# Kernel optimization log

Hardware: AMD Instinct MI355X
Metric: run time of the kernel (lower is better)

Reference implementation:

```python
import jax, jax.numpy as jnp
import numpy as np

D_MODEL = 1024
D_FF = 1024
NUM_EXPERTS = 8
TOP_K = 2


def setup_inputs() -> dict:
    key = jax.random.key(0)
    ks = jax.random.split(key, 5)
    s_in = 1.0 / np.sqrt(D_MODEL)
    s_ff = 1.0 / np.sqrt(D_FF)
    return {
        "x": jax.random.normal(ks[0], (4, 2048, D_MODEL), dtype=jnp.float32),
        "gate_w": jax.random.normal(ks[1], (NUM_EXPERTS, D_MODEL), dtype=jnp.float32) * s_in,
        # torch Linear weight layout: [out_features, in_features], stacked over experts
        "w_gate": jax.random.normal(ks[2], (NUM_EXPERTS, D_FF, D_MODEL), dtype=jnp.float32) * s_in,
        "w_up": jax.random.normal(ks[3], (NUM_EXPERTS, D_FF, D_MODEL), dtype=jnp.float32) * s_in,
        "w_down": jax.random.normal(ks[4], (NUM_EXPERTS, D_MODEL, D_FF), dtype=jnp.float32) * s_ff,
    }


def reference(x, gate_w, w_gate, w_up, w_down):
    B, S, D = x.shape
    T = B * S
    E = gate_w.shape[0]
    xt = x.reshape(T, D)

    # Router
    logits = xt @ gate_w.T                      # [T, E]
    probs = jax.nn.softmax(logits, axis=-1)
    top_v, top_i = jax.lax.top_k(probs, TOP_K)  # [T, K]
    top_v = top_v / jnp.sum(top_v, axis=-1, keepdims=True)

    tokens_per_expert = jnp.sum(jax.nn.one_hot(top_i, E, dtype=jnp.float32), axis=(0, 1))  # [E]
    f = tokens_per_expert / jnp.sum(tokens_per_expert)
    P = jnp.mean(probs, axis=0)
    aux_loss = E * jnp.sum(f * P)

    # Combine weights: per-token weight for each expert (sum over top-k slots)
    combine = jnp.zeros((T, E), dtype=x.dtype).at[jnp.arange(T)[:, None], top_i].add(top_v)  # [T, E]

    # Dense per-expert SwiGLU (equivalent math to masked gather/scatter loop)
    g = jnp.einsum('td,efd->etf', xt, w_gate)   # [E, T, F]
    u = jnp.einsum('td,efd->etf', xt, w_up)     # [E, T, F]
    act = jax.nn.silu(g) * u
    eo = jnp.einsum('etf,edf->etd', act, w_down)  # [E, T, D]

    out = jnp.einsum('te,etd->td', combine, eo).reshape(B, S, D)
    return out, aux_loss, tokens_per_expert
```

## Files before the change

### kernel.cpp

```cpp
#include <hip/hip_runtime.h>


#define T_TOK   8192
#define DM      1024
#define DFF     1024
#define NE      8
#define CAP     16384
#define R1_BLK  (T_TOK / 4)
#define CVT_BLK 2048

typedef __attribute__((ext_vector_type(8))) short bf16x8;
typedef __attribute__((ext_vector_type(4))) float f32x4;

#define ASYNC16(gp, lp) __builtin_amdgcn_global_load_lds( \
    (const __attribute__((address_space(1))) unsigned int*)(gp), \
    (__attribute__((address_space(3))) unsigned int*)(lp), 16, 0, 0)

__device__ __forceinline__ unsigned short f2bf(float f) {
    union { float f; unsigned u; } c; c.f = f;
    unsigned r = c.u + 0x7fffu + ((c.u >> 16) & 1u);
    return (unsigned short)(r >> 16);
}
__device__ __forceinline__ float bf2f(unsigned short h) {
    union { unsigned u; float f; } c; c.u = ((unsigned)h) << 16;
    return c.f;
}

__global__ __launch_bounds__(256) void pre_kernel(
    const float* __restrict__ x, const float* __restrict__ gate_w,
    const float* __restrict__ s0, const float* __restrict__ s1, const float* __restrict__ s2,
    unsigned short* __restrict__ d0, unsigned short* __restrict__ d1, unsigned short* __restrict__ d2,
    unsigned short* __restrict__ xb,
    int* __restrict__ topi, float2* __restrict__ topw, float* __restrict__ psum_part)
{
    int tid = threadIdx.x;

    if (blockIdx.x >= R1_BLK) {
        int base = (blockIdx.x - R1_BLK) * 256 + tid;
        #pragma unroll
        for (int it = 0; it < 12; ++it) {
            int idx = base + it * (CVT_BLK * 256);
            int seg = idx >> 21;
            int off = (idx & ((1 << 21) - 1)) * 4;
            const float* s = (seg == 0) ? s0 : (seg == 1) ? s1 : s2;
            unsigned short* d = (seg == 0) ? d0 : (seg == 1) ? d1 : d2;
            float4 v = *(const float4*)(s + off);
            ushort4 o;
            o.x = f2bf(v.x); o.y = f2bf(v.y); o.z = f2bf(v.z); o.w = f2bf(v.w);
            *(ushort4*)(d + off) = o;
        }
        return;
    }

    __shared__ float gw[NE * DM];
    __shared__ float blk_psum[NE];

    for (int i = tid; i < NE * DM; i += 256) gw[i] = gate_w[i];
    if (tid < NE) blk_psum[tid] = 0.f;
    __syncthreads();

    int wv = tid >> 6, lane = tid & 63;
    int t = blockIdx.x * 4 + wv;

    float acc[NE];
    #pragma unroll
    for (int e = 0; e < NE; ++e) acc[e] = 0.f;
    const float* xr = x + (size_t)t * DM;
    unsigned short* xbr = xb + (size_t)t * DM;
    #pragma unroll 4
    for (int i = 0; i < DM / 64; ++i) {
        float xv = xr[i * 64 + lane];
        xbr[i * 64 + lane] = f2bf(xv);
        #pragma unroll
        for (int e = 0; e < NE; ++e)
            acc[e] += xv * gw[e * DM + i * 64 + lane];
    }
    #pragma unroll
    for (int e = 0; e < NE; ++e) {
        float v = acc[e];
        #pragma unroll
        for (int s = 32; s > 0; s >>= 1) v += __shfl_xor(v, s, 64);
        acc[e] = v;
    }
    if (lane == 0) {
        float mx = acc[0];
        #pragma unroll
        for (int e = 1; e < NE; ++e) mx = fmaxf(mx, acc[e]);
        float p[NE], sum = 0.f;
        #pragma unroll
        for (int e = 0; e < NE; ++e) { p[e] = expf(acc[e] - mx); sum += p[e]; }
        float inv = 1.f / sum;
        #pragma unroll
        for (int e = 0; e < NE; ++e) { p[e] *= inv; atomicAdd(&blk_psum[e], p[e]); }
        int i1 = 0; float v1 = p[0];
        #pragma unroll
        for (int e = 1; e < NE; ++e) if (p[e] > v1) { v1 = p[e]; i1 = e; }
        int i2 = -1; float v2 = -1.f;
        #pragma unroll
        for (int e = 0; e < NE; ++e) { if (e == i1) continue; if (p[e] > v2) { v2 = p[e]; i2 = e; } }
        float winv = 1.f / (v1 + v2);
        topi[t] = i1 | (i2 << 8);
        topw[t] = make_float2(v1 * winv, v2 * winv);
    }
    __syncthreads();
    if (tid < NE) psum_part[blockIdx.x * NE + tid] = blk_psum[tid];
}

__global__ __launch_bounds__(1024) void scatfin_kernel(
    const int* __restrict__ topi, const float* __restrict__ psum_part,
    int* __restrict__ elist, int* __restrict__ ecnt, float* __restrict__ out_tail)
{
    __shared__ int lcnt[NE], rbase[NE], cb8[NE];
    __shared__ float parts[NE];
    __shared__ float red[1024];
    int tid = threadIdx.x;

    if (tid < NE) rbase[tid] = 0;
    __syncthreads();
    #pragma unroll
    for (int ch = 0; ch < T_TOK / 1024; ++ch) {
        int tt = ch * 1024 + tid;
        int pk = topi[tt];
        int e1 = pk & 0xff, e2 = (pk >> 8) & 0xff;
        if (tid < NE) lcnt[tid] = 0;
        __syncthreads();
        int p1 = atomicAdd(&lcnt[e1], 1);
        int p2 = atomicAdd(&lcnt[e2], 1);
        __syncthreads();
        if (tid < NE) { cb8[tid] = rbase[tid]; rbase[tid] += lcnt[tid]; }
        __syncthreads();
        elist[e1 * CAP + cb8[e1] + p1] = tt * 2 + 0;
        elist[e2 * CAP + cb8[e2] + p2] = tt * 2 + 1;
        __syncthreads();
    }
    if (tid < NE) ecnt[tid] = rbase[tid];

    int e = tid & 7, b0 = tid >> 3;
    float s = 0.f;
    for (int b = b0; b < R1_BLK; b += 128) s += psum_part[b * NE + e];
    red[tid] = s;
    __syncthreads();
    if (tid < NE) {
        float tot = 0.f;
        #pragma unroll
        for (int j = 0; j < 128; ++j) tot += red[tid + NE * j];
        float P = tot / (float)T_TOK;
        float f = (float)rbase[tid] / (float)(2 * T_TOK);
        parts[tid] = f * P;
        out_tail[1 + tid] = (float)rbase[tid];
    }
    __syncthreads();
    if (tid == 0) {
        float s2 = 0.f;
        for (int i = 0; i < NE; ++i) s2 += parts[i];
        out_tail[0] = (float)NE * s2;
    }
}

__global__ __launch_bounds__(256) void gemm1_kernel(
    const unsigned short* __restrict__ xb,
    const unsigned short* __restrict__ wgb,
    const unsigned short* __restrict__ wub,
    const int* __restrict__ elist, const int* __restrict__ ecnt,
    unsigned short* __restrict__ Hbuf)
{
    int e = blockIdx.z, mt = blockIdx.y, ft = blockIdx.x;
    int ne = ecnt[e];
    if (mt * 128 >= ne) return;

    __shared__ unsigned short As[128 * 64];
    __shared__ unsigned short Gs[64 * 64];
    __shared__ unsigned short Us[64 * 64];
    __shared__ int tsafe[128];
    __shared__ int rawts[128];

    int tid = threadIdx.x;
    if (tid < 128) {
        int pos = mt * 128 + tid;
        int ts0 = elist[e * CAP + mt * 128];
        int ts = (pos < ne) ? elist[e * CAP + pos] : ts0;
        tsafe[tid] = ts >> 1;
        rawts[tid] = (pos < ne) ? ts : -1;
    }
    __syncthreads();

    int wave = tid >> 6, lane = tid & 63;
    int quad = lane >> 4, col = lane & 15;
    int cr = tid >> 3;
    int cl = ((tid & 7) ^ (cr & 7)) * 8;

    const size_t woff = (size_t)e * (size_t)DFF * DM;
    const unsigned short* ap[4];
    #pragma unroll
    for (int j = 0; j < 4; ++j) ap[j] = xb + (size_t)tsafe[j * 32 + cr] * DM + cl;
    const unsigned short* gp[2];
    const unsigned short* up[2];
    #pragma unroll
    for (int j = 0; j < 2; ++j) {
        gp[j] = wgb + woff + (size_t)(ft * 64 + j * 32 + cr) * DM + cl;
        up[j] = wub + woff + (size_t)(ft * 64 + j * 32 + cr) * DM + cl;
    }
    unsigned short* lA = As + wave * 512;
    unsigned short* lG = Gs + wave * 512;
    unsigned short* lU = Us + wave * 512;

    f32x4 accG[2][4], accU[2][4];
    #pragma unroll
    for (int i = 0; i < 2; ++i)
        #pragma unroll
        for (int n = 0; n < 4; ++n) { accG[i][n] = (f32x4){0,0,0,0}; accU[i][n] = (f32x4){0,0,0,0}; }

    for (int k0 = 0; k0 < DM; k0 += 64) {
        __syncthreads();
        #pragma unroll
        for (int j = 0; j < 4; ++j) ASYNC16(ap[j] + k0, lA + j * 2048);
        #pragma unroll
        for (int j = 0; j < 2; ++j) {
            ASYNC16(gp[j] + k0, lG + j * 2048);
            ASYNC16(up[j] + k0, lU + j * 2048);
        }
        __syncthreads();
        #pragma unroll
        for (int ksoff = 0; ksoff < 8; ksoff += 4) {
            bf16x8 a[2], g[4], u[4];
            #pragma unroll
            for (int i = 0; i < 2; ++i) {
                int m = wave * 32 + i * 16 + col;
                a[i] = *(const bf16x8*)&As[m * 64 + ((quad + ksoff) ^ (m & 7)) * 8];
            }
            #pragma unroll
            for (int n = 0; n < 4; ++n) {
                int nb = n * 16 + col;
                int off = nb * 64 + ((quad + ksoff) ^ (nb & 7)) * 8;
                g[n] = *(const bf16x8*)&Gs[off];
                u[n] = *(const bf16x8*)&Us[off];
            }
            #pragma unroll
            for (int i = 0; i < 2; ++i)
                #pragma unroll
                for (int n = 0; n < 4; ++n) {
                    accG[i][n] = __builtin_amdgcn_mfma_f32_16x16x32_bf16(a[i], g[n], accG[i][n], 0, 0, 0);
                    accU[i][n] = __builtin_amdgcn_mfma_f32_16x16x32_bf16(a[i], u[n], accU[i][n], 0, 0, 0);
                }
        }
    }
    #pragma unroll
    for (int i = 0; i < 2; ++i) {
        #pragma unroll
        for (int r = 0; r < 4; ++r) {
            int row = wave * 32 + i * 16 + quad * 4 + r;
            int ts = rawts[row];
            if (ts < 0) continue;
            unsigned short* hr = Hbuf + (size_t)ts * DFF + ft * 64 + col;
            #pragma unroll
            for (int n = 0; n < 4; ++n) {
                float gg = accG[i][n][r], uu = accU[i][n][r];
                float h = (gg / (1.f + expf(-gg))) * uu;
                hr[n * 16] = f2bf(h);
            }
        }
    }
}

__global__ __launch_bounds__(256) void gemm2_kernel(
    const unsigned short* __restrict__ Hbuf,
    const unsigned short* __restrict__ wdb,
    const int* __restrict__ elist, const int* __restrict__ ecnt,
    unsigned short* __restrict__ eo)
{
    int e = blockIdx.z, mt = blockIdx.y, dt = blockIdx.x;
    int ne = ecnt[e];
    if (mt * 128 >= ne) return;

    __shared__ unsigned short As[128 * 64];
    __shared__ unsigned short Bs[128 * 64];
    __shared__ int tsafe[128];
    __shared__ int rawts[128];

    int tid = threadIdx.x;
    if (tid < 128) {
        int pos = mt * 128 + tid;
        int ts0 = elist[e * CAP + mt * 128];
        int ts = (pos < ne) ? elist[e * CAP + pos] : ts0;
        tsafe[tid] = ts;
        rawts[tid] = (pos < ne) ? ts : -1;
    }
    __syncthreads();

    int wave = tid >> 6, lane = tid & 63;
    int quad = lane >> 4, col = lane & 15;
    int wr = (wave >> 1) * 64, wc = (wave & 1) * 64;
    int cr = tid >> 3;
    int cl = ((tid & 7) ^ (cr & 7)) * 8;

    const size_t woff = (size_t)e * (size_t)DM * DFF;
    const unsigned short* ap[4];
    const unsigned short* bp[4];
    #pragma unroll
    for (int j = 0; j < 4; ++j) {
        ap[j] = Hbuf + (size_t)tsafe[j * 32 + cr] * DFF + cl;
        bp[j] = wdb + woff + (size_t)(dt * 128 + j * 32 + cr) * DFF + cl;
    }
    unsigned short* lA = As + wave * 512;
    unsigned short* lB = Bs + wave * 512;

    f32x4 acc[4][4];
    #pragma unroll
    for (int i = 0; i < 4; ++i)
        #pragma unroll
        for (int n = 0; n < 4; ++n) acc[i][n] = (f32x4){0,0,0,0};

    for (int k0 = 0; k0 < DFF; k0 += 64) {
        __syncthreads();
        #pragma unroll
        for (int j = 0; j < 4; ++j) {
            ASYNC16(ap[j] + k0, lA + j * 2048);
            ASYNC16(bp[j] + k0, lB + j * 2048);
        }
        __syncthreads();
        #pragma unroll
        for (int ksoff = 0; ksoff < 8; ksoff += 4) {
            bf16x8 a[4], b[4];
            #pragma unroll
            for (int i = 0; i < 4; ++i) {
                int m = wr + i * 16 + col;
                a[i] = *(const bf16x8*)&As[m * 64 + ((quad + ksoff) ^ (m & 7)) * 8];
            }
            #pragma unroll
            for (int n = 0; n < 4; ++n) {
                int nb = wc + n * 16 + col;
                b[n] = *(const bf16x8*)&Bs[nb * 64 + ((quad + ksoff) ^ (nb & 7)) * 8];
            }
            #pragma unroll
            for (int i = 0; i < 4; ++i)
                #pragma unroll
                for (int n = 0; n < 4; ++n)
                    acc[i][n] = __builtin_amdgcn_mfma_f32_16x16x32_bf16(a[i], b[n], acc[i][n], 0, 0, 0);
        }
    }
    #pragma unroll
    for (int i = 0; i < 4; ++i) {
        #pragma unroll
        for (int r = 0; r < 4; ++r) {
            int row = wr + i * 16 + quad * 4 + r;
            int ts = rawts[row];
            if (ts < 0) continue;
            unsigned short* er = eo + (size_t)ts * DM + dt * 128 + wc + col;
            #pragma unroll
            for (int n = 0; n < 4; ++n)
                er[n * 16] = f2bf(acc[i][n][r]);
        }
    }
}

__global__ __launch_bounds__(256) void combine_kernel(
    const unsigned short* __restrict__ eo, const float2* __restrict__ topw,
    float* __restrict__ out)
{
    int idx = blockIdx.x * 256 + threadIdx.x;
    int t = idx >> 7;
    int c = (idx & 127) << 3;
    float2 w = topw[t];
    const unsigned short* e0 = eo + (size_t)(t * 2) * DM + c;
    ushort4 a0 = *(const ushort4*)e0;
    ushort4 a1 = *(const ushort4*)(e0 + 4);
    ushort4 b0 = *(const ushort4*)(e0 + DM);
    ushort4 b1 = *(const ushort4*)(e0 + DM + 4);
    float* orow = out + (size_t)t * DM + c;
    float4 o0, o1;
    o0.x = w.x * bf2f(a0.x) + w.y * bf2f(b0.x);
    o0.y = w.x * bf2f(a0.y) + w.y * bf2f(b0.y);
    o0.z = w.x * bf2f(a0.z) + w.y * bf2f(b0.z);
    o0.w = w.x * bf2f(a0.w) + w.y * bf2f(b0.w);
    o1.x = w.x * bf2f(a1.x) + w.y * bf2f(b1.x);
    o1.y = w.x * bf2f(a1.y) + w.y * bf2f(b1.y);
    o1.z = w.x * bf2f(a1.z) + w.y * bf2f(b1.z);
    o1.w = w.x * bf2f(a1.w) + w.y * bf2f(b1.w);
    *(float4*)orow = o0;
    *(float4*)(orow + 4) = o1;
}

extern "C" void kernel_launch(void* const* d_in, const int* in_sizes, int n_in,
                              void* d_out, int out_size, void* d_ws, size_t ws_size,
                              hipStream_t stream) {
    const float* x      = (const float*)d_in[0];
    const float* gate_w = (const float*)d_in[1];
    const float* w_gate = (const float*)d_in[2];
    const float* w_up   = (const float*)d_in[3];
    const float* w_down = (const float*)d_in[4];
    float* out = (float*)d_out;

    char* p = (char*)d_ws;
    unsigned short* xb   = (unsigned short*)p; p += (size_t)T_TOK * DM * 2;
    unsigned short* wgb  = (unsigned short*)p; p += (size_t)NE * DFF * DM * 2;
    unsigned short* wub  = (unsigned short*)p; p += (size_t)NE * DFF * DM * 2;
    unsigned short* wdb  = (unsigned short*)p; p += (size_t)NE * DM * DFF * 2;
    unsigned short* Hbuf = (unsigned short*)p; p += (size_t)2 * T_TOK * DFF * 2;
    int*   elist = (int*)p;   p += (size_t)NE * CAP * 4;
    int*   ecnt  = (int*)p;   p += NE * 4;
    int*   topi  = (int*)p;   p += (size_t)T_TOK * 4;
    float2* topw = (float2*)p; p += (size_t)T_TOK * 8;
    float* psum_part = (float*)p; p += (size_t)R1_BLK * NE * 4;
    unsigned short* eo = wgb;

    pre_kernel<<<R1_BLK + CVT_BLK, 256, 0, stream>>>(
        x, gate_w, w_gate, w_up, w_down, wgb, wub, wdb,
        xb, topi, topw, psum_part);
    scatfin_kernel<<<1, 1024, 0, stream>>>(topi, psum_part, elist, ecnt,
                                           out + (size_t)T_TOK * DM);
    gemm1_kernel<<<dim3(DFF / 64, CAP / 128, NE), 256, 0, stream>>>(xb, wgb, wub, elist, ecnt, Hbuf);
    gemm2_kernel<<<dim3(DM / 128, CAP / 128, NE), 256, 0, stream>>>(Hbuf, wdb, elist, ecnt, eo);
    combine_kernel<<<T_TOK * DM / 8 / 256, 256, 0, stream>>>(eo, topw, out);
}
```

Baseline: 347.5 us.

## Store expert-sorted rows contiguously so gemm2 reads H without gather

The hidden activations and expert outputs are now laid out in expert-sorted order with per-expert base offsets, instead of indexed by token-slot. gemm2 can then read its A rows contiguously with no per-block index load. combine gathers through a new per-token row index instead. The pre-kernel also interleaves router blocks with weight-conversion blocks so the two kinds of work run concurrently rather than as two separate phases. The cost is an extra pass in the single-block scatter kernel and scattered reads in combine.

```diff
diff --git a/kernel.cpp b/kernel.cpp
--- a/kernel.cpp
+++ b/kernel.cpp
@@ -5,8 +5,8 @@
 #define DM      1024
 #define DFF     1024
 #define NE      8
-#define CAP     16384
-#define R1_BLK  (T_TOK / 4)
+#define TOTS    (2 * T_TOK)
+#define R1_BLK  2048
 #define CVT_BLK 2048
 
 typedef __attribute__((ext_vector_type(8))) short bf16x8;
@@ -34,9 +34,10 @@
     int* __restrict__ topi, float2* __restrict__ topw, float* __restrict__ psum_part)
 {
     int tid = threadIdx.x;
-
-    if (blockIdx.x >= R1_BLK) {
-        int base = (blockIdx.x - R1_BLK) * 256 + tid;
+    int sub = blockIdx.x >> 1;
+
+    if (blockIdx.x & 1) {
+        int base = sub * 256 + tid;
         #pragma unroll
         for (int it = 0; it < 12; ++it) {
             int idx = base + it * (CVT_BLK * 256);
@@ -60,7 +61,7 @@
     __syncthreads();
 
     int wv = tid >> 6, lane = tid & 63;
-    int t = blockIdx.x * 4 + wv;
+    int t = sub * 4 + wv;
 
     float acc[NE];
     #pragma unroll
@@ -103,19 +104,20 @@
         topw[t] = make_float2(v1 * winv, v2 * winv);
     }
     __syncthreads();
-    if (tid < NE) psum_part[blockIdx.x * NE + tid] = blk_psum[tid];
+    if (tid < NE) psum_part[sub * NE + tid] = blk_psum[tid];
 }
 
 __global__ __launch_bounds__(1024) void scatfin_kernel(
     const int* __restrict__ topi, const float* __restrict__ psum_part,
-    int* __restrict__ elist, int* __restrict__ ecnt, float* __restrict__ out_tail)
+    int* __restrict__ elist, int2* __restrict__ cidx,
+    int* __restrict__ ecnt, int* __restrict__ ebaseg, float* __restrict__ out_tail)
 {
-    __shared__ int lcnt[NE], rbase[NE], cb8[NE];
+    __shared__ int lcnt[NE], run[NE], cb[NE], ebase[NE];
     __shared__ float parts[NE];
     __shared__ float red[1024];
     int tid = threadIdx.x;
 
-    if (tid < NE) rbase[tid] = 0;
+    if (tid < NE) run[tid] = 0;
     __syncthreads();
     #pragma unroll
     for (int ch = 0; ch < T_TOK / 1024; ++ch) {
@@ -127,13 +129,28 @@
         int p1 = atomicAdd(&lcnt[e1], 1);
         int p2 = atomicAdd(&lcnt[e2], 1);
         __syncthreads();
-        if (tid < NE) { cb8[tid] = rbase[tid]; rbase[tid] += lcnt[tid]; }
-        __syncthreads();
-        elist[e1 * CAP + cb8[e1] + p1] = tt * 2 + 0;
-        elist[e2 * CAP + cb8[e2] + p2] = tt * 2 + 1;
-        __syncthreads();
-    }
-    if (tid < NE) ecnt[tid] = rbase[tid];
+        if (tid < NE) { cb[tid] = run[tid]; run[tid] += lcnt[tid]; }
+        __syncthreads();
+        cidx[tt] = make_int2(cb[e1] + p1, cb[e2] + p2);
+    }
+    __syncthreads();
+    if (tid == 0) {
+        int s = 0;
+        for (int e = 0; e < NE; ++e) { ebase[e] = s; s += run[e]; }
+    }
+    __syncthreads();
+    #pragma unroll
+    for (int ch = 0; ch < T_TOK / 1024; ++ch) {
+        int tt = ch * 1024 + tid;
+        int pk = topi[tt];
+        int e1 = pk & 0xff, e2 = (pk >> 8) & 0xff;
+        int2 pp = cidx[tt];
+        int r1 = ebase[e1] + pp.x, r2 = ebase[e2] + pp.y;
+        elist[r1] = tt;
+        elist[r2] = tt;
+        cidx[tt] = make_int2(r1, r2);
+    }
+    if (tid < NE) { ecnt[tid] = run[tid]; ebaseg[tid] = ebase[tid]; }
 
     int e = tid & 7, b0 = tid >> 3;
     float s = 0.f;
@@ -145,9 +162,9 @@
         #pragma unroll
         for (int j = 0; j < 128; ++j) tot += red[tid + NE * j];
         float P = tot / (float)T_TOK;
-        float f = (float)rbase[tid] / (float)(2 * T_TOK);
+        float f = (float)run[tid] / (float)(2 * T_TOK);
         parts[tid] = f * P;
-        out_tail[1 + tid] = (float)rbase[tid];
+        out_tail[1 + tid] = (float)run[tid];
     }
     __syncthreads();
     if (tid == 0) {
@@ -162,25 +179,23 @@
     const unsigned short* __restrict__ wgb,
     const unsigned short* __restrict__ wub,
     const int* __restrict__ elist, const int* __restrict__ ecnt,
+    const int* __restrict__ ebaseg,
     unsigned short* __restrict__ Hbuf)
 {
     int e = blockIdx.z, mt = blockIdx.y, ft = blockIdx.x;
     int ne = ecnt[e];
     if (mt * 128 >= ne) return;
+    int base = ebaseg[e];
 
     __shared__ unsigned short As[128 * 64];
     __shared__ unsigned short Gs[64 * 64];
     __shared__ unsigned short Us[64 * 64];
-    __shared__ int tsafe[128];
-    __shared__ int rawts[128];
+    __shared__ int tok[128];
 
     int tid = threadIdx.x;
     if (tid < 128) {
-        int pos = mt * 128 + tid;
-        int ts0 = elist[e * CAP + mt * 128];
-        int ts = (pos < ne) ? elist[e * CAP + pos] : ts0;
-        tsafe[tid] = ts >> 1;
-        rawts[tid] = (pos < ne) ? ts : -1;
+        int slot = base + mt * 128 + tid;
+        tok[tid] = elist[min(slot, TOTS - 1)];
     }
     __syncthreads();
 
@@ -192,7 +207,7 @@
     const size_t woff = (size_t)e * (size_t)DFF * DM;
     const unsigned short* ap[4];
     #pragma unroll
-    for (int j = 0; j < 4; ++j) ap[j] = xb + (size_t)tsafe[j * 32 + cr] * DM + cl;
+    for (int j = 0; j < 4; ++j) ap[j] = xb + (size_t)tok[j * 32 + cr] * DM + cl;
     const unsigned short* gp[2];
     const unsigned short* up[2];
     #pragma unroll
@@ -248,10 +263,9 @@
     for (int i = 0; i < 2; ++i) {
         #pragma unroll
         for (int r = 0; r < 4; ++r) {
-            int row = wave * 32 + i * 16 + quad * 4 + r;
-            int ts = rawts[row];
-            if (ts < 0) continue;
-            unsigned short* hr = Hbuf + (size_t)ts * DFF + ft * 64 + col;
+            int pos = mt * 128 + wave * 32 + i * 16 + quad * 4 + r;
+            if (pos >= ne) continue;
+            unsigned short* hr = Hbuf + (size_t)(base + pos) * DFF + ft * 64 + col;
             #pragma unroll
             for (int n = 0; n < 4; ++n) {
                 float gg = accG[i][n][r], uu = accU[i][n][r];
@@ -265,28 +279,18 @@
 __global__ __launch_bounds__(256) void gemm2_kernel(
     const unsigned short* __restrict__ Hbuf,
     const unsigned short* __restrict__ wdb,
-    const int* __restrict__ elist, const int* __restrict__ ecnt,
+    const int* __restrict__ ecnt, const int* __restrict__ ebaseg,
     unsigned short* __restrict__ eo)
 {
     int e = blockIdx.z, mt = blockIdx.y, dt = blockIdx.x;
     int ne = ecnt[e];
     if (mt * 128 >= ne) return;
+    int base = ebaseg[e];
 
     __shared__ unsigned short As[128 * 64];
     __shared__ unsigned short Bs[128 * 64];
-    __shared__ int tsafe[128];
-    __shared__ int rawts[128];
 
     int tid = threadIdx.x;
-    if (tid < 128) {
-        int pos = mt * 128 + tid;
-        int ts0 = elist[e * CAP + mt * 128];
-        int ts = (pos < ne) ? elist[e * CAP + pos] : ts0;
-        tsafe[tid] = ts;
-        rawts[tid] = (pos < ne) ? ts : -1;
-    }
-    __syncthreads();
-
     int wave = tid >> 6, lane = tid & 63;
     int quad = lane >> 4, col = lane & 15;
     int wr = (wave >> 1) * 64, wc = (wave & 1) * 64;
@@ -298,7 +302,8 @@
     const unsigned short* bp[4];
     #pragma unroll
     for (int j = 0; j < 4; ++j) {
-        ap[j] = Hbuf + (size_t)tsafe[j * 32 + cr] * DFF + cl;
+        int hrow = min(base + mt * 128 + j * 32 + cr, TOTS - 1);
+        ap[j] = Hbuf + (size_t)hrow * DFF + cl;
         bp[j] = wdb + woff + (size_t)(dt * 128 + j * 32 + cr) * DFF + cl;
     }
     unsigned short* lA = As + wave * 512;
@@ -342,10 +347,9 @@
     for (int i = 0; i < 4; ++i) {
         #pragma unroll
         for (int r = 0; r < 4; ++r) {
-            int row = wr + i * 16 + quad * 4 + r;
-            int ts = rawts[row];
-            if (ts < 0) continue;
-            unsigned short* er = eo + (size_t)ts * DM + dt * 128 + wc + col;
+            int pos = mt * 128 + wr + i * 16 + quad * 4 + r;
+            if (pos >= ne) continue;
+            unsigned short* er = eo + (size_t)(base + pos) * DM + dt * 128 + wc + col;
             #pragma unroll
             for (int n = 0; n < 4; ++n)
                 er[n * 16] = f2bf(acc[i][n][r]);
@@ -355,17 +359,19 @@
 
 __global__ __launch_bounds__(256) void combine_kernel(
     const unsigned short* __restrict__ eo, const float2* __restrict__ topw,
-    float* __restrict__ out)
+    const int2* __restrict__ cidx, float* __restrict__ out)
 {
     int idx = blockIdx.x * 256 + threadIdx.x;
     int t = idx >> 7;
     int c = (idx & 127) << 3;
     float2 w = topw[t];
-    const unsigned short* e0 = eo + (size_t)(t * 2) * DM + c;
-    ushort4 a0 = *(const ushort4*)e0;
-    ushort4 a1 = *(const ushort4*)(e0 + 4);
-    ushort4 b0 = *(const ushort4*)(e0 + DM);
-    ushort4 b1 = *(const ushort4*)(e0 + DM + 4);
+    int2 rr = cidx[t];
+    const unsigned short* p0 = eo + (size_t)rr.x * DM + c;
+    const unsigned short* p1 = eo + (size_t)rr.y * DM + c;
+    ushort4 a0 = *(const ushort4*)p0;
+    ushort4 a1 = *(const ushort4*)(p0 + 4);
+    ushort4 b0 = *(const ushort4*)p1;
+    ushort4 b1 = *(const ushort4*)(p1 + 4);
     float* orow = out + (size_t)t * DM + c;
     float4 o0, o1;
     o0.x = w.x * bf2f(a0.x) + w.y * bf2f(b0.x);
@@ -395,20 +401,24 @@
     unsigned short* wgb  = (unsigned short*)p; p += (size_t)NE * DFF * DM * 2;
     unsigned short* wub  = (unsigned short*)p; p += (size_t)NE * DFF * DM * 2;
     unsigned short* wdb  = (unsigned short*)p; p += (size_t)NE * DM * DFF * 2;
-    unsigned short* Hbuf = (unsigned short*)p; p += (size_t)2 * T_TOK * DFF * 2;
-    int*   elist = (int*)p;   p += (size_t)NE * CAP * 4;
+    unsigned short* Hbuf = (unsigned short*)p; p += (size_t)TOTS * DFF * 2;
+    int*   elist = (int*)p;   p += (size_t)TOTS * 4;
     int*   ecnt  = (int*)p;   p += NE * 4;
+    int*   ebaseg= (int*)p;   p += NE * 4;
     int*   topi  = (int*)p;   p += (size_t)T_TOK * 4;
     float2* topw = (float2*)p; p += (size_t)T_TOK * 8;
+    int2*  cidx  = (int2*)p;  p += (size_t)T_TOK * 8;
     float* psum_part = (float*)p; p += (size_t)R1_BLK * NE * 4;
     unsigned short* eo = wgb;
 
     pre_kernel<<<R1_BLK + CVT_BLK, 256, 0, stream>>>(
         x, gate_w, w_gate, w_up, w_down, wgb, wub, wdb,
         xb, topi, topw, psum_part);
-    scatfin_kernel<<<1, 1024, 0, stream>>>(topi, psum_part, elist, ecnt,
+    scatfin_kernel<<<1, 1024, 0, stream>>>(topi, psum_part, elist, cidx, ecnt, ebaseg,
                                            out + (size_t)T_TOK * DM);
-    gemm1_kernel<<<dim3(DFF / 64, CAP / 128, NE), 256, 0, stream>>>(xb, wgb, wub, elist, ecnt, Hbuf);
-    gemm2_kernel<<<dim3(DM / 128, CAP / 128, NE), 256, 0, stream>>>(Hbuf, wdb, elist, ecnt, eo);
-    combine_kernel<<<T_TOK * DM / 8 / 256, 256, 0, stream>>>(eo, topw, out);
-}
+    gemm1_kernel<<<dim3(DFF / 64, TOTS / 128, NE), 256, 0, stream>>>(
+        xb, wgb, wub, elist, ecnt, ebaseg, Hbuf);
+    gemm2_kernel<<<dim3(DM / 128, TOTS / 128, NE), 256, 0, stream>>>(
+        Hbuf, wdb, ecnt, ebaseg, eo);
+    combine_kernel<<<T_TOK * DM / 8 / 256, 256, 0, stream>>>(eo, topw, cidx, out);
+}
```

Measured after the change: 334.7 us. 3.7% less time.
